# Performance work log

Hardware: AMD Instinct MI355X
Metric: run time of the kernel (lower is better)

The kernel has to match this reference:

```python
import jax, jax.numpy as jnp
import numpy as np

BIG = 1e10  # sentinel for masked-out (padded) points, like pytorch3d's masking


def setup_inputs() -> dict:
    key = jax.random.key(0)
    k1, k2, k3, k4 = jax.random.split(key, 4)
    B, N, M = 16, 4096, 4096
    source_cloud = jax.random.normal(k1, (B, N, 2), dtype=jnp.float32)
    target_cloud = jax.random.normal(k2, (B, M, 2), dtype=jnp.float32)
    source_mask = jax.random.randint(k3, (B,), 0, N)  # lengths1
    target_mask = jax.random.randint(k4, (B,), 0, M)  # lengths2
    return {
        "source_cloud": source_cloud,
        "target_cloud": target_cloud,
        "source_mask": source_mask,
        "target_mask": target_mask,
    }


def reference(source_cloud, target_cloud, source_mask, target_mask):
    # source_cloud: [B, N, 2], target_cloud: [B, M, 2]
    # source_mask/target_mask: int lengths [B] (knn_points lengths1/lengths2)
    B, N, _ = source_cloud.shape
    M = target_cloud.shape[1]

    s2 = jnp.sum(source_cloud * source_cloud, axis=-1)  # [B, N]
    t2 = jnp.sum(target_cloud * target_cloud, axis=-1)  # [B, M]
    # squared pairwise distances [B, N, M]
    d2 = (s2[:, :, None] + t2[:, None, :]
          - 2.0 * jnp.einsum('bnd,bmd->bnm', source_cloud, target_cloud))

    src_valid = jnp.arange(N)[None, :] < source_mask[:, None]  # [B, N]
    tgt_valid = jnp.arange(M)[None, :] < target_mask[:, None]  # [B, M]

    # forward: for each source point, 1-NN over valid target points
    d2_fwd = jnp.where(tgt_valid[:, None, :], d2, BIG)
    min_fwd = jnp.maximum(jnp.min(d2_fwd, axis=-1), 0.0)  # [B, N]
    # backward: for each target point, 1-NN over valid source points
    d2_bwd = jnp.where(src_valid[:, :, None], d2, BIG)
    min_bwd = jnp.maximum(jnp.min(d2_bwd, axis=-2), 0.0)  # [B, M]

    # padded query points get dist 0 (pytorch3d knn_points semantics), then sqrt
    chamfer_forward = jnp.where(src_valid, jnp.sqrt(min_fwd), 0.0)
    chamfer_backward = jnp.where(tgt_valid, jnp.sqrt(min_bwd), 0.0)
    return (chamfer_forward, chamfer_backward)
```

## Files before the change

kernel.cpp:

```cpp
#include <hip/hip_runtime.h>


#define NQ 16
typedef float f2 __attribute__((ext_vector_type(2)));

__global__ __launch_bounds__(256, 2) void chamfer_main(
    const float* __restrict__ src, const float* __restrict__ tgt,
    const int* __restrict__ slen, const int* __restrict__ tlen,
    float* __restrict__ part)
{
    __shared__ float4 sh_xy[64];
    __shared__ f2     sh_n[64];

    const int g   = blockIdx.x;
    const int tid = threadIdx.x;

    int row = -1, pc = 0, Lp = 0, acc = 0;
    #pragma unroll
    for (int rr = 0; rr < 32; ++rr) {
        const int L = (rr < 16) ? tlen[rr] : slen[rr - 16];
        const int n = (L + 127) >> 7;
        if (row < 0 && g < acc + n) { row = rr; pc = g - acc; Lp = L; }
        acc += n;
    }
    if (row < 0) return;
    const int dir = row >> 4, b = row & 15;

    const float* Q = dir ? tgt : src;
    const float* P = dir ? src : tgt;

    if (tid < 64) {
        const int base = pc * 128 + tid * 2;
        const float4 pp = ((const float4*)P)[(b * 4096 + base) >> 1];
        const float n0 = (base + 0 < Lp) ? fmaf(pp.x, pp.x, pp.y * pp.y) : 1e30f;
        const float n1 = (base + 1 < Lp) ? fmaf(pp.z, pp.z, pp.w * pp.w) : 1e30f;
        sh_xy[tid] = make_float4(pp.x, pp.z, pp.y, pp.w);
        sh_n[tid]  = f2{n0, n1};
    }
    __syncthreads();

    float mx[NQ], my[NQ], s2[NQ], best[NQ];
    #pragma unroll
    for (int k = 0; k < NQ; ++k) {
        const float2 q = ((const float2*)Q)[b * 4096 + tid + k * 256];
        mx[k] = -2.f * q.x;
        my[k] = -2.f * q.y;
        s2[k] = fmaf(q.x, q.x, q.y * q.y);
        best[k] = 3.0e38f;
    }

    #pragma unroll 4
    for (int j = 0; j < 64; ++j) {
        const float4 xy = sh_xy[j];
        const f2 xp = f2{xy.x, xy.y};
        const f2 yp = f2{xy.z, xy.w};
        const f2 np = sh_n[j];
        #pragma unroll
        for (int k = 0; k < NQ; ++k) {
            f2 v = xp * mx[k] + np;
            v = yp * my[k] + v;
            best[k] = fminf(best[k], fminf(v.x, v.y));
        }
    }

    float* slice = part + ((size_t)row * 32 + pc) * 4096;
    #pragma unroll
    for (int k = 0; k < NQ; ++k)
        slice[tid + k * 256] = fmaxf(best[k] + s2[k], 0.f);
}

__global__ __launch_bounds__(128) void chamfer_reduce(
    const float* __restrict__ part,
    const int* __restrict__ slen, const int* __restrict__ tlen,
    float* __restrict__ out)
{
    const int t  = blockIdx.x * 128 + threadIdx.x;
    const int i4 = t * 4;
    const int row = i4 >> 12;
    const int dir = row >> 4, b = row & 15;
    const int i   = i4 & 4095;
    const int Lq = dir ? tlen[b] : slen[b];
    const int Lp = dir ? slen[b] : tlen[b];
    const int nact = (Lp + 127) >> 7;

    float4 best = make_float4(1e10f, 1e10f, 1e10f, 1e10f);
    const float4* p = (const float4*)(part + (size_t)row * 32 * 4096 + i);
    #pragma unroll 4
    for (int s = 0; s < nact; ++s) {
        const float4 v = p[(size_t)s * 1024];
        best.x = fminf(best.x, v.x);
        best.y = fminf(best.y, v.y);
        best.z = fminf(best.z, v.z);
        best.w = fminf(best.w, v.w);
    }
    float4 r;
    r.x = (i + 0 < Lq) ? sqrtf(best.x) : 0.f;
    r.y = (i + 1 < Lq) ? sqrtf(best.y) : 0.f;
    r.z = (i + 2 < Lq) ? sqrtf(best.z) : 0.f;
    r.w = (i + 3 < Lq) ? sqrtf(best.w) : 0.f;
    ((float4*)out)[t] = r;
}

extern "C" void kernel_launch(void* const* d_in, const int* in_sizes, int n_in,
                              void* d_out, int out_size, void* d_ws, size_t ws_size,
                              hipStream_t stream) {
    const float* src = (const float*)d_in[0];
    const float* tgt = (const float*)d_in[1];
    const int* slen  = (const int*)d_in[2];
    const int* tlen  = (const int*)d_in[3];
    float* part = (float*)d_ws;

    chamfer_main<<<1024, 256, 0, stream>>>(src, tgt, slen, tlen, part);
    chamfer_reduce<<<256, 128, 0, stream>>>(part, slen, tlen, (float*)d_out);
}
```

Baseline: 83.96 us.

## Fuse chamfer partial-min and reduce into one query-tiled kernel

The two-kernel scheme, which split target points across blocks and wrote per-chunk partial minima to a workspace before reducing, is replaced by a single kernel. Each block now owns 128 queries, one per thread, and loops over every valid target point through 512-pair shared-memory chunks. Query tiles lying entirely past the valid length write zeros and exit early. This removes the partial-buffer traffic, the second launch, and the work spent on padded queries. In exchange each thread holds only one query, so every shared-memory read feeds less arithmetic, and per-block work varies with the point lengths.

```diff
diff --git a/kernel.cpp b/kernel.cpp
--- a/kernel.cpp
+++ b/kernel.cpp
@@ -1,104 +1,76 @@
 #include <hip/hip_runtime.h>
 
 
-#define NQ 16
+#define CHP 512
 typedef float f2 __attribute__((ext_vector_type(2)));
 
-__global__ __launch_bounds__(256, 2) void chamfer_main(
+__global__ __launch_bounds__(128) void chamfer_fused(
     const float* __restrict__ src, const float* __restrict__ tgt,
     const int* __restrict__ slen, const int* __restrict__ tlen,
-    float* __restrict__ part)
+    float* __restrict__ out)
 {
-    __shared__ float4 sh_xy[64];
-    __shared__ f2     sh_n[64];
+    __shared__ float4 sh_xy[CHP];
+    __shared__ f2     sh_n[CHP];
 
     const int g   = blockIdx.x;
     const int tid = threadIdx.x;
+    const int row = g & 31;
+    const int qc  = g >> 5;
+    const int dir = row >> 4, b = row & 15;
 
-    int row = -1, pc = 0, Lp = 0, acc = 0;
-    #pragma unroll
-    for (int rr = 0; rr < 32; ++rr) {
-        const int L = (rr < 16) ? tlen[rr] : slen[rr - 16];
-        const int n = (L + 127) >> 7;
-        if (row < 0 && g < acc + n) { row = rr; pc = g - acc; Lp = L; }
-        acc += n;
+    const int Lq = dir ? tlen[b] : slen[b];
+    const int Lp = dir ? slen[b] : tlen[b];
+
+    const int q = qc * 128 + tid;
+    float* op = out + row * 4096;
+
+    if (qc * 128 >= Lq) {
+        op[q] = 0.f;
+        return;
     }
-    if (row < 0) return;
-    const int dir = row >> 4, b = row & 15;
 
     const float* Q = dir ? tgt : src;
     const float* P = dir ? src : tgt;
 
-    if (tid < 64) {
-        const int base = pc * 128 + tid * 2;
-        const float4 pp = ((const float4*)P)[(b * 4096 + base) >> 1];
-        const float n0 = (base + 0 < Lp) ? fmaf(pp.x, pp.x, pp.y * pp.y) : 1e30f;
-        const float n1 = (base + 1 < Lp) ? fmaf(pp.z, pp.z, pp.w * pp.w) : 1e30f;
-        sh_xy[tid] = make_float4(pp.x, pp.z, pp.y, pp.w);
-        sh_n[tid]  = f2{n0, n1};
-    }
-    __syncthreads();
+    const float2 qv = ((const float2*)Q)[b * 4096 + q];
+    const float mx = -2.f * qv.x;
+    const float my = -2.f * qv.y;
+    const float s2 = fmaf(qv.x, qv.x, qv.y * qv.y);
+    float best = 1e10f;
 
-    float mx[NQ], my[NQ], s2[NQ], best[NQ];
-    #pragma unroll
-    for (int k = 0; k < NQ; ++k) {
-        const float2 q = ((const float2*)Q)[b * 4096 + tid + k * 256];
-        mx[k] = -2.f * q.x;
-        my[k] = -2.f * q.y;
-        s2[k] = fmaf(q.x, q.x, q.y * q.y);
-        best[k] = 3.0e38f;
-    }
+    const int npair = (Lp + 1) >> 1;
+    const float4* Pp = (const float4*)P + b * 2048;
 
-    #pragma unroll 4
-    for (int j = 0; j < 64; ++j) {
-        const float4 xy = sh_xy[j];
-        const f2 xp = f2{xy.x, xy.y};
-        const f2 yp = f2{xy.z, xy.w};
-        const f2 np = sh_n[j];
+    for (int c0 = 0; c0 < npair; c0 += CHP) {
+        const int npc = min(CHP, npair - c0);
+        __syncthreads();
         #pragma unroll
-        for (int k = 0; k < NQ; ++k) {
-            f2 v = xp * mx[k] + np;
-            v = yp * my[k] + v;
-            best[k] = fminf(best[k], fminf(v.x, v.y));
+        for (int i = 0; i < 4; ++i) {
+            const int p = tid + i * 128;
+            if (p < npc) {
+                const float4 pp = Pp[c0 + p];
+                const int i0 = (c0 + p) * 2;
+                const float n0 = (i0 + 0 < Lp) ? fmaf(pp.x, pp.x, pp.y * pp.y) : 1e30f;
+                const float n1 = (i0 + 1 < Lp) ? fmaf(pp.z, pp.z, pp.w * pp.w) : 1e30f;
+                sh_xy[p] = make_float4(pp.x, pp.z, pp.y, pp.w);
+                sh_n[p]  = f2{n0, n1};
+            }
+        }
+        __syncthreads();
+
+        #pragma unroll 8
+        for (int j = 0; j < npc; ++j) {
+            const float4 xy = sh_xy[j];
+            const f2 np = sh_n[j];
+            const f2 xp = f2{xy.x, xy.y};
+            const f2 yp = f2{xy.z, xy.w};
+            f2 v = xp * mx + np;
+            v = yp * my + v;
+            best = fminf(best, fminf(v.x, v.y));
         }
     }
 
-    float* slice = part + ((size_t)row * 32 + pc) * 4096;
-    #pragma unroll
-    for (int k = 0; k < NQ; ++k)
-        slice[tid + k * 256] = fmaxf(best[k] + s2[k], 0.f);
-}
-
-__global__ __launch_bounds__(128) void chamfer_reduce(
-    const float* __restrict__ part,
-    const int* __restrict__ slen, const int* __restrict__ tlen,
-    float* __restrict__ out)
-{
-    const int t  = blockIdx.x * 128 + threadIdx.x;
-    const int i4 = t * 4;
-    const int row = i4 >> 12;
-    const int dir = row >> 4, b = row & 15;
-    const int i   = i4 & 4095;
-    const int Lq = dir ? tlen[b] : slen[b];
-    const int Lp = dir ? slen[b] : tlen[b];
-    const int nact = (Lp + 127) >> 7;
-
-    float4 best = make_float4(1e10f, 1e10f, 1e10f, 1e10f);
-    const float4* p = (const float4*)(part + (size_t)row * 32 * 4096 + i);
-    #pragma unroll 4
-    for (int s = 0; s < nact; ++s) {
-        const float4 v = p[(size_t)s * 1024];
-        best.x = fminf(best.x, v.x);
-        best.y = fminf(best.y, v.y);
-        best.z = fminf(best.z, v.z);
-        best.w = fminf(best.w, v.w);
-    }
-    float4 r;
-    r.x = (i + 0 < Lq) ? sqrtf(best.x) : 0.f;
-    r.y = (i + 1 < Lq) ? sqrtf(best.y) : 0.f;
-    r.z = (i + 2 < Lq) ? sqrtf(best.z) : 0.f;
-    r.w = (i + 3 < Lq) ? sqrtf(best.w) : 0.f;
-    ((float4*)out)[t] = r;
+    op[q] = (q < Lq) ? sqrtf(fmaxf(best + s2, 0.f)) : 0.f;
 }
 
 extern "C" void kernel_launch(void* const* d_in, const int* in_sizes, int n_in,
@@ -108,8 +80,7 @@
     const float* tgt = (const float*)d_in[1];
     const int* slen  = (const int*)d_in[2];
     const int* tlen  = (const int*)d_in[3];
-    float* part = (float*)d_ws;
+    (void)d_ws; (void)ws_size;
 
-    chamfer_main<<<1024, 256, 0, stream>>>(src, tgt, slen, tlen, part);
-    chamfer_reduce<<<256, 128, 0, stream>>>(part, slen, tlen, (float*)d_out);
+    chamfer_fused<<<1024, 128, 0, stream>>>(src, tgt, slen, tlen, (float*)d_out);
 }
```

Measured after the change: 99.58 us. 1.19x slower.
